# Kernel tuning notes

Measured on AMD Instinct MI355X. Metric: run time of the kernel, lower is better.

## Reference

```python
import jax, jax.numpy as jnp
import numpy as np

N_NODES, N_EDGES, F_IN = 8192, 32768, 16
N_SUB, N_GRAPH = 512, 32
EDGE_DIM, HID = 5, 128
DIMS = [(16, 32), (32, 64), (64, 64)]  # (M_in, M_out) per NNConv layer


def _segment_mean(x, seg, n):
    s = jax.ops.segment_sum(x, seg, num_segments=n)
    c = jax.ops.segment_sum(jnp.ones((x.shape[0], 1), x.dtype), seg, num_segments=n)
    return s / jnp.maximum(c, 1.0)


def _nnconv(x, src, dst, eattr, W1, b1, W2, b2, root, bias):
    # edge MLP -> per-edge weight matrix theta: [E, M_in, M_out]
    h = jax.nn.relu(eattr @ W1 + b1)
    theta = (h @ W2 + b2).reshape(-1, x.shape[1], root.shape[1])
    msg = jnp.einsum('ei,eio->eo', x[src], theta)          # gather + per-edge matvec
    agg = jax.ops.segment_sum(msg, dst, num_segments=x.shape[0])  # scatter-add (aggr='add')
    return agg + x @ root + bias


def setup_inputs() -> dict:
    key = jax.random.key(0)
    ks = jax.random.split(key, 32)
    inp = {}
    inp['x'] = jax.random.normal(ks[0], (N_NODES, F_IN), jnp.float32)
    inp['edge_index'] = jax.random.randint(ks[1], (2, N_EDGES), 0, N_NODES)
    inp['edge_attr'] = jax.random.uniform(ks[2], (N_EDGES, EDGE_DIM), jnp.float32)
    inp['node_to_subgraph'] = jnp.sort(jax.random.randint(ks[3], (N_NODES,), 0, N_SUB))
    inp['subgraph_to_graph'] = jnp.sort(jax.random.randint(ks[4], (N_SUB,), 0, N_GRAPH))
    i = 5
    for l, (ci, co) in enumerate(DIMS):
        inp[f'W1_{l}'] = jax.random.normal(ks[i], (EDGE_DIM, HID), jnp.float32) * 0.1
        inp[f'b1_{l}'] = jnp.zeros((HID,), jnp.float32)
        inp[f'W2_{l}'] = jax.random.normal(ks[i + 1], (HID, ci * co), jnp.float32) * 0.05
        inp[f'b2_{l}'] = jnp.zeros((ci * co,), jnp.float32)
        inp[f'root_{l}'] = jax.random.normal(ks[i + 2], (ci, co), jnp.float32) * 0.1
        inp[f'bias_{l}'] = jnp.zeros((co,), jnp.float32)
        i += 3
    inp['fc1_w'] = jax.random.normal(ks[i], (64, 32), jnp.float32) * 0.1
    inp['fc1_b'] = jnp.zeros((32,), jnp.float32)
    inp['fc2_w'] = jax.random.normal(ks[i + 1], (32, 16), jnp.float32) * 0.1
    inp['fc2_b'] = jnp.zeros((16,), jnp.float32)
    inp['fc3_w'] = jax.random.normal(ks[i + 2], (16, 1), jnp.float32) * 0.1
    inp['fc3_b'] = jnp.zeros((1,), jnp.float32)
    return inp


def reference(x, edge_index, edge_attr, node_to_subgraph, subgraph_to_graph,
              W1_0, b1_0, W2_0, b2_0, root_0, bias_0,
              W1_1, b1_1, W2_1, b2_1, root_1, bias_1,
              W1_2, b1_2, W2_2, b2_2, root_2, bias_2,
              fc1_w, fc1_b, fc2_w, fc2_b, fc3_w, fc3_b):
    src, dst = edge_index[0], edge_index[1]
    layers = [(W1_0, b1_0, W2_0, b2_0, root_0, bias_0),
              (W1_1, b1_1, W2_1, b2_1, root_1, bias_1),
              (W1_2, b1_2, W2_2, b2_2, root_2, bias_2)]
    h = x
    for (W1, b1, W2, b2, root, bias) in layers:
        h = jax.nn.elu(_nnconv(h, src, dst, edge_attr, W1, b1, W2, b2, root, bias))
    h = _segment_mean(h, node_to_subgraph, N_SUB)      # global_mean_pool over subgraphs
    h = _segment_mean(h, subgraph_to_graph, N_GRAPH)   # global_mean_pool over graphs
    h = jax.nn.elu(h @ fc1_w + fc1_b)
    h = jax.nn.elu(h @ fc2_w + fc2_b)
    return (h @ fc3_w + fc3_b).reshape(-1)
```

## Files before the change

### kernel.cpp

```cpp
#include <hip/hip_runtime.h>

#define E_EDGES 32768
#define NN 8192
#define HID 128

typedef _Float16 half8 __attribute__((ext_vector_type(8)));
typedef _Float16 half4 __attribute__((ext_vector_type(4)));
typedef float f32x4 __attribute__((ext_vector_type(4)));

__device__ __forceinline__ void prep_one(int idx, int l2ci, int l2co,
                                         const float* __restrict__ W2,
                                         const float* __restrict__ b2,
                                         _Float16* __restrict__ out) {
  int CI = 1 << l2ci, CO = 1 << l2co;
  int Kmain = CI << 7;
  int j = idx & 7;
  int n = (idx >> 3) & (CO - 1);
  int kg = idx >> (3 + l2co);
  int k = kg * 8 + j;
  float v = 0.f;
  if (k < Kmain) {
    int hh = k >> l2ci, i = k & (CI - 1);
    v = W2[((hh << l2ci) + i) * CO + n];
  } else if (k < Kmain + CI) {
    v = b2[(k - Kmain) * CO + n];
  }
  out[idx] = (_Float16)v;
}

#define ZTOT (8192 * 32 + 8192 * 64 + 8192 * 64 + 512 * 64 + 512)
#define PREP0 (2176 * 32)
#define PREP1 (4224 * 64)
#define PREP2 (8320 * 64)

__global__ void prep_k(float* __restrict__ zr,
                       const float* __restrict__ W2a, const float* __restrict__ b2a, _Float16* __restrict__ oa,
                       const float* __restrict__ W2b, const float* __restrict__ b2b, _Float16* __restrict__ ob,
                       const float* __restrict__ W2c, const float* __restrict__ b2c, _Float16* __restrict__ oc) {
  int idx = blockIdx.x * 256 + threadIdx.x;
  if (idx < ZTOT) { zr[idx] = 0.f; return; }
  idx -= ZTOT;
  if (idx < PREP0) prep_one(idx, 4, 5, W2a, b2a, oa);
  else if (idx < PREP0 + PREP1) prep_one(idx - PREP0, 5, 6, W2b, b2b, ob);
  else if (idx < PREP0 + PREP1 + PREP2) prep_one(idx - PREP0 - PREP1, 6, 6, W2c, b2c, oc);
}

template <int CI, int CO>
__launch_bounds__(256, 4)
__global__ void msg_mfma_k(const float* __restrict__ xcur, const int* __restrict__ src,
                           const int* __restrict__ dst, const float* __restrict__ eattr,
                           const float* __restrict__ W1, const float* __restrict__ b1,
                           const _Float16* __restrict__ Bsw, float* __restrict__ agg) {
  constexpr int ME = 128;
  constexpr int L2CI = (CI == 64) ? 6 : ((CI == 32) ? 5 : 4);
  constexpr int XSTR = CI + 8;
  constexpr int FC = CO / 16;
  constexpr int C4 = CI / 4;
  constexpr int L2C4 = L2CI - 2;
  constexpr int NV = (CI == 64) ? 2 : 1;
  constexpr int HS = 40;
  constexpr int CW = CI / 4;
  constexpr int NP = CW / 2;

  __shared__ _Float16 he_t[ME * HS];
  __shared__ _Float16 xs_s[ME * XSTR];
  __shared__ float ea_s[ME * 5];
  __shared__ float W1s[5 * 32];
  __shared__ float b1s[32];
  __shared__ int src_s[ME];
  __shared__ int dst_s[ME];

  int t = threadIdx.x;
  int e0 = blockIdx.x * ME;
  int y = blockIdx.y;
  int hbeg = y * 32;

  for (int j = t; j < ME * 5; j += 256) ea_s[j] = eattr[e0 * 5 + j];
  if (t < 5 * 32) W1s[t] = W1[(t >> 5) * HID + hbeg + (t & 31)];
  if (t < 32) b1s[t] = b1[hbeg + t];
  if (t < ME) { src_s[t] = src[e0 + t]; dst_s[t] = dst[e0 + t]; }
  __syncthreads();

  for (int j = t; j < 32 * ME; j += 256) {
    int hl = j >> 7, e = j & (ME - 1);
    float v = b1s[hl];
#pragma unroll
    for (int d = 0; d < 5; ++d) v += ea_s[e * 5 + d] * W1s[d * 32 + hl];
    he_t[e * HS + hl] = (_Float16)fmaxf(v, 0.f);
  }
  for (int j = t; j < ME * C4; j += 256) {
    int e = j >> L2C4, i4 = j & (C4 - 1);
    float4 v = ((const float4*)xcur)[src_s[e] * C4 + i4];
    half4 hq = {(_Float16)v.x, (_Float16)v.y, (_Float16)v.z, (_Float16)v.w};
    *(half4*)&xs_s[e * XSTR + i4 * 4] = hq;
  }
  __syncthreads();

  int lane = t & 63;
  int w = t >> 6;
  int quad = lane >> 4, l15 = lane & 15;
  int hsel = (quad >> 1) & 1;

  half8 xreg[2][NV];
#pragma unroll
  for (int fr = 0; fr < 2; ++fr)
#pragma unroll
    for (int v = 0; v < NV; ++v)
      xreg[fr][v] = *(const half8*)&xs_s[(w * 32 + fr * 16 + l15) * XSTR +
                                         ((quad * 8 + v * 32) & (CI - 1))];

  int cbeg = y * CI;
  int TC = CI + ((y == 3) ? 4 : 0);

  const half8* bsw8 = (const half8*)Bsw;
  int ib = quad * CO + l15;

  f32x4 acc[2][FC];
#pragma unroll
  for (int fr = 0; fr < 2; ++fr)
#pragma unroll
    for (int fc = 0; fc < FC; ++fc)
#pragma unroll
      for (int r = 0; r < 4; ++r) acc[fr][fc][r] = 0.f;

  half8 breg[2][FC];
#pragma unroll
  for (int p = 0; p < 2; ++p)
#pragma unroll
    for (int fc = 0; fc < FC; ++fc)
      breg[p][fc] = bsw8[(cbeg + p) * 4 * CO + ib + fc * 16];

  for (int win = 0; win < 4; ++win) {
    half8 hreg[2];
#pragma unroll
    for (int fr = 0; fr < 2; ++fr)
      hreg[fr] = *(const half8*)&he_t[(w * 32 + fr * 16 + l15) * HS + win * 8];
    for (int cl2 = 0; cl2 < NP; ++cl2) {
#pragma unroll
      for (int p = 0; p < 2; ++p) {
        int cl = win * CW + cl2 * 2 + p;
        int vi = (CI == 64) ? p : 0;
        half8 a[2];
#pragma unroll
        for (int fr = 0; fr < 2; ++fr) {
          _Float16 hv;
          if (CI == 16)      hv = hreg[fr][2 * (cl2 * 2 + p) + hsel];
          else if (CI == 32) hv = hreg[fr][cl2 * 2 + p];
          else               hv = hreg[fr][cl2];
          half8 hb = {hv, hv, hv, hv, hv, hv, hv, hv};
          a[fr] = xreg[fr][vi] * hb;
        }
#pragma unroll
        for (int fc = 0; fc < FC; ++fc) {
#pragma unroll
          for (int fr = 0; fr < 2; ++fr)
            acc[fr][fc] = __builtin_amdgcn_mfma_f32_16x16x32_f16(a[fr], breg[p][fc], acc[fr][fc], 0, 0, 0);
        }
        int cn = cl + 2;
        if (cn >= TC) cn = TC - 1;
#pragma unroll
        for (int fc = 0; fc < FC; ++fc)
          breg[p][fc] = bsw8[(cbeg + cn) * 4 * CO + ib + fc * 16];
      }
    }
  }

  if (y == 3) {
#pragma unroll
    for (int j = 0; j < 4; ++j) {
      int cl = CI + j;
      int p = j & 1;
      int vi = (CI == 64) ? p : 0;
#pragma unroll
      for (int fc = 0; fc < FC; ++fc) {
#pragma unroll
        for (int fr = 0; fr < 2; ++fr)
          acc[fr][fc] = __builtin_amdgcn_mfma_f32_16x16x32_f16(xreg[fr][vi], breg[p][fc], acc[fr][fc], 0, 0, 0);
      }
      int cn = cl + 2;
      if (cn >= TC) cn = TC - 1;
#pragma unroll
      for (int fc = 0; fc < FC; ++fc)
        breg[p][fc] = bsw8[(cbeg + cn) * 4 * CO + ib + fc * 16];
    }
  }

#pragma unroll
  for (int fr = 0; fr < 2; ++fr)
#pragma unroll
    for (int r = 0; r < 4; ++r) {
      int el = w * 32 + fr * 16 + quad * 4 + r;
      int d = dst_s[el];
      float* base = agg + (size_t)d * CO + l15;
#pragma unroll
      for (int fc = 0; fc < FC; ++fc)
        atomicAdd(base + fc * 16, acc[fr][fc][r]);
    }
}

template <int CI, int CO, bool POOL, bool CNT>
__global__ void fin_k(const float* __restrict__ xcur, const float* __restrict__ root,
                      const float* __restrict__ bias, const float* __restrict__ agg,
                      const int* __restrict__ n2s, int* __restrict__ cnt_sub,
                      float* __restrict__ ssum, float* __restrict__ xnext) {
  constexpr int NB = 256 / CO;
  __shared__ float xs[NB * CI];
  int t = threadIdx.x;
  int n0 = blockIdx.x * NB;
  for (int j = t; j < NB * CI; j += 256) xs[j] = xcur[n0 * CI + j];
  __syncthreads();
  int nl = t / CO, o = t & (CO - 1);
  int n = n0 + nl;
  float a = bias[o] + agg[n * CO + o];
#pragma unroll
  for (int i = 0; i < CI; ++i) a += xs[nl * CI + i] * root[i * CO + o];
  float r = a > 0.f ? a : expm1f(a);
  if (CNT && o == 0) atomicAdd(&cnt_sub[n2s[n]], 1);
  if (POOL) atomicAdd(&ssum[(n2s[n] << 6) + o], r);
  else xnext[n * CO + o] = r;
}

__device__ __forceinline__ int lbound(const int* __restrict__ a, int n, int v) {
  int lo = 0, hi = n;
  while (lo < hi) { int m = (lo + hi) >> 1; if (a[m] < v) lo = m + 1; else hi = m; }
  return lo;
}

__global__ void head_k(const float* __restrict__ ssum, const int* __restrict__ cnt_sub,
                       const int* __restrict__ s2g,
                       const float* __restrict__ w1, const float* __restrict__ b1,
                       const float* __restrict__ w2, const float* __restrict__ b2,
                       const float* __restrict__ w3, const float* __restrict__ b3,
                       float* __restrict__ out) {
  int g = blockIdx.x;
  int t = threadIdx.x;
  __shared__ float m[64], s1[32], s2[16];
  int slo = lbound(s2g, 512, g);
  int shi = lbound(s2g, 512, g + 1);
  float acc = 0.f;
  for (int s = slo; s < shi; ++s)
    acc += ssum[(s << 6) + t] / fmaxf((float)cnt_sub[s], 1.f);
  m[t] = acc / fmaxf((float)(shi - slo), 1.f);
  __syncthreads();
  if (t < 32) {
    float a = b1[t];
    for (int i = 0; i < 64; ++i) a += m[i] * w1[i * 32 + t];
    s1[t] = a > 0.f ? a : expm1f(a);
  }
  __syncthreads();
  if (t < 16) {
    float a = b2[t];
    for (int i = 0; i < 32; ++i) a += s1[i] * w2[i * 16 + t];
    s2[t] = a > 0.f ? a : expm1f(a);
  }
  __syncthreads();
  if (t == 0) {
    float a = b3[0];
    for (int i = 0; i < 16; ++i) a += s2[i] * w3[i];
    out[g] = a;
  }
}

extern "C" void kernel_launch(void* const* d_in, const int* in_sizes, int n_in,
                              void* d_out, int out_size, void* d_ws, size_t ws_size,
                              hipStream_t stream) {
  (void)in_sizes; (void)n_in; (void)out_size; (void)ws_size;
  const float* x0 = (const float*)d_in[0];
  const int* ei = (const int*)d_in[1];
  const float* ea = (const float*)d_in[2];
  const int* n2s = (const int*)d_in[3];
  const int* s2g = (const int*)d_in[4];
  const float* W1_[3] = {(const float*)d_in[5], (const float*)d_in[11], (const float*)d_in[17]};
  const float* b1_[3] = {(const float*)d_in[6], (const float*)d_in[12], (const float*)d_in[18]};
  const float* W2_[3] = {(const float*)d_in[7], (const float*)d_in[13], (const float*)d_in[19]};
  const float* b2_[3] = {(const float*)d_in[8], (const float*)d_in[14], (const float*)d_in[20]};
  const float* rt_[3] = {(const float*)d_in[9], (const float*)d_in[15], (const float*)d_in[21]};
  const float* bs_[3] = {(const float*)d_in[10], (const float*)d_in[16], (const float*)d_in[22]};
  const float* fc1w = (const float*)d_in[23]; const float* fc1b = (const float*)d_in[24];
  const float* fc2w = (const float*)d_in[25]; const float* fc2b = (const float*)d_in[26];
  const float* fc3w = (const float*)d_in[27]; const float* fc3b = (const float*)d_in[28];
  float* out = (float*)d_out;

  const int* srcp = ei;
  const int* dstp = ei + E_EDGES;

  char* wsb = (char*)d_ws;
  size_t off = 0;
  auto alloc = [&](size_t bytes) {
    void* p = wsb + off;
    off += (bytes + 255) & ~(size_t)255;
    return p;
  };
  _Float16* Bsw0 = (_Float16*)alloc((size_t)PREP0 * 2);
  _Float16* Bsw1 = (_Float16*)alloc((size_t)PREP1 * 2);
  _Float16* Bsw2 = (_Float16*)alloc((size_t)PREP2 * 2);
  float* agg1 = (float*)alloc((size_t)NN * 32 * 4);
  float* agg2 = (float*)alloc((size_t)NN * 64 * 4);
  float* agg3 = (float*)alloc((size_t)NN * 64 * 4);
  float* ssum = (float*)alloc((size_t)512 * 64 * 4);
  int* cnt_sub = (int*)alloc((size_t)512 * 4);
  float* x1 = (float*)alloc((size_t)NN * 32 * 4);
  float* x2 = (float*)alloc((size_t)NN * 64 * 4);

  const int preptot = ZTOT + PREP0 + PREP1 + PREP2;
  prep_k<<<(preptot + 255) / 256, 256, 0, stream>>>(agg1, W2_[0], b2_[0], Bsw0,
                                                    W2_[1], b2_[1], Bsw1,
                                                    W2_[2], b2_[2], Bsw2);

  dim3 mg(E_EDGES / 128, 4);
  msg_mfma_k<16, 32><<<mg, 256, 0, stream>>>(x0, srcp, dstp, ea, W1_[0], b1_[0], Bsw0, agg1);
  fin_k<16, 32, false, true><<<NN / 8, 256, 0, stream>>>(x0, rt_[0], bs_[0], agg1, n2s, cnt_sub, ssum, x1);
  msg_mfma_k<32, 64><<<mg, 256, 0, stream>>>(x1, srcp, dstp, ea, W1_[1], b1_[1], Bsw1, agg2);
  fin_k<32, 64, false, false><<<NN / 4, 256, 0, stream>>>(x1, rt_[1], bs_[1], agg2, n2s, cnt_sub, ssum, x2);
  msg_mfma_k<64, 64><<<mg, 256, 0, stream>>>(x2, srcp, dstp, ea, W1_[2], b1_[2], Bsw2, agg3);
  fin_k<64, 64, true, false><<<NN / 4, 256, 0, stream>>>(x2, rt_[2], bs_[2], agg3, n2s, cnt_sub, ssum, nullptr);

  head_k<<<32, 64, 0, stream>>>(ssum, cnt_sub, s2g, fc1w, fc1b, fc2w, fc2b, fc3w, fc3b, out);
}
```

Measured before the change: 281.6 us.

## Enlarge per-block edge tile to 512 and restage B layout per split

```diff
diff --git a/kernel.cpp b/kernel.cpp
--- a/kernel.cpp
+++ b/kernel.cpp
@@ -5,33 +5,37 @@
 #define HID 128
 
 typedef _Float16 half8 __attribute__((ext_vector_type(8)));
-typedef _Float16 half4 __attribute__((ext_vector_type(4)));
 typedef float f32x4 __attribute__((ext_vector_type(4)));
 
-__device__ __forceinline__ void prep_one(int idx, int l2ci, int l2co,
+#define S0 (4 * 22 * 1024)
+#define S1 (4 * 38 * 2048)
+#define S2 (4 * 70 * 2048)
+#define ZTOT (8192 * 32 + 8192 * 64 + 8192 * 64 + 512 * 64 + 512)
+
+__device__ __forceinline__ void prep_one(int idx, int l2ci, int l2co, int tcp2,
                                          const float* __restrict__ W2,
                                          const float* __restrict__ b2,
                                          _Float16* __restrict__ out) {
   int CI = 1 << l2ci, CO = 1 << l2co;
-  int Kmain = CI << 7;
-  int j = idx & 7;
-  int n = (idx >> 3) & (CO - 1);
-  int kg = idx >> (3 + l2co);
-  int k = kg * 8 + j;
+  int CH = 32 * CO;
+  int per_split = tcp2 * CH;
+  int y = idx / per_split;
+  int r = idx - y * per_split;
+  int cl = r / CH;
+  int m = r & (CH - 1);
+  int j = m & 7, l15 = (m >> 3) & 15, quad = (m >> 7) & 3, fc = m >> 9;
+  int kl = cl * 32 + quad * 8 + j;
+  int n = fc * 16 + l15;
+  int kmain = 32 * CI;
   float v = 0.f;
-  if (k < Kmain) {
-    int hh = k >> l2ci, i = k & (CI - 1);
-    v = W2[((hh << l2ci) + i) * CO + n];
-  } else if (k < Kmain + CI) {
-    v = b2[(k - Kmain) * CO + n];
+  if (kl < kmain) {
+    int h = y * 32 + (kl >> l2ci), i = kl & (CI - 1);
+    v = W2[(h * CI + i) * CO + n];
+  } else if (y == 3 && kl < kmain + CI) {
+    v = b2[(kl - kmain) * CO + n];
   }
   out[idx] = (_Float16)v;
 }
-
-#define ZTOT (8192 * 32 + 8192 * 64 + 8192 * 64 + 512 * 64 + 512)
-#define PREP0 (2176 * 32)
-#define PREP1 (4224 * 64)
-#define PREP2 (8320 * 64)
 
 __global__ void prep_k(float* __restrict__ zr,
                        const float* __restrict__ W2a, const float* __restrict__ b2a, _Float16* __restrict__ oa,
@@ -40,30 +44,28 @@
   int idx = blockIdx.x * 256 + threadIdx.x;
   if (idx < ZTOT) { zr[idx] = 0.f; return; }
   idx -= ZTOT;
-  if (idx < PREP0) prep_one(idx, 4, 5, W2a, b2a, oa);
-  else if (idx < PREP0 + PREP1) prep_one(idx - PREP0, 5, 6, W2b, b2b, ob);
-  else if (idx < PREP0 + PREP1 + PREP2) prep_one(idx - PREP0 - PREP1, 6, 6, W2c, b2c, oc);
+  if (idx < S0) { prep_one(idx, 4, 5, 22, W2a, b2a, oa); return; }
+  idx -= S0;
+  if (idx < S1) { prep_one(idx, 5, 6, 38, W2b, b2b, ob); return; }
+  idx -= S1;
+  if (idx < S2) prep_one(idx, 6, 6, 70, W2c, b2c, oc);
 }
 
 template <int CI, int CO>
-__launch_bounds__(256, 4)
+__launch_bounds__(256, 1)
 __global__ void msg_mfma_k(const float* __restrict__ xcur, const int* __restrict__ src,
                            const int* __restrict__ dst, const float* __restrict__ eattr,
                            const float* __restrict__ W1, const float* __restrict__ b1,
                            const _Float16* __restrict__ Bsw, float* __restrict__ agg) {
-  constexpr int ME = 128;
-  constexpr int L2CI = (CI == 64) ? 6 : ((CI == 32) ? 5 : 4);
-  constexpr int XSTR = CI + 8;
+  constexpr int ME = 512;
   constexpr int FC = CO / 16;
-  constexpr int C4 = CI / 4;
-  constexpr int L2C4 = L2CI - 2;
+  constexpr int CH8 = 4 * CO;
+  constexpr int TCP = (CI == 64) ? 68 : ((CI == 32) ? 36 : 20);
+  constexpr int CW = (CI == 64) ? 16 : ((CI == 32) ? 8 : 4);
   constexpr int NV = (CI == 64) ? 2 : 1;
   constexpr int HS = 40;
-  constexpr int CW = CI / 4;
-  constexpr int NP = CW / 2;
-
-  __shared__ _Float16 he_t[ME * HS];
-  __shared__ _Float16 xs_s[ME * XSTR];
+
+  __shared__ __align__(16) _Float16 he_t[ME * HS];
   __shared__ float ea_s[ME * 5];
   __shared__ float W1s[5 * 32];
   __shared__ float b1s[32];
@@ -76,120 +78,113 @@
   int hbeg = y * 32;
 
   for (int j = t; j < ME * 5; j += 256) ea_s[j] = eattr[e0 * 5 + j];
-  if (t < 5 * 32) W1s[t] = W1[(t >> 5) * HID + hbeg + (t & 31)];
+  if (t < 160) W1s[t] = W1[(t >> 5) * HID + hbeg + (t & 31)];
   if (t < 32) b1s[t] = b1[hbeg + t];
-  if (t < ME) { src_s[t] = src[e0 + t]; dst_s[t] = dst[e0 + t]; }
+  src_s[t] = src[e0 + t]; src_s[t + 256] = src[e0 + 256 + t];
+  dst_s[t] = dst[e0 + t]; dst_s[t + 256] = dst[e0 + 256 + t];
   __syncthreads();
 
   for (int j = t; j < 32 * ME; j += 256) {
-    int hl = j >> 7, e = j & (ME - 1);
+    int hl = j >> 9, e = j & (ME - 1);
     float v = b1s[hl];
 #pragma unroll
     for (int d = 0; d < 5; ++d) v += ea_s[e * 5 + d] * W1s[d * 32 + hl];
     he_t[e * HS + hl] = (_Float16)fmaxf(v, 0.f);
-  }
-  for (int j = t; j < ME * C4; j += 256) {
-    int e = j >> L2C4, i4 = j & (C4 - 1);
-    float4 v = ((const float4*)xcur)[src_s[e] * C4 + i4];
-    half4 hq = {(_Float16)v.x, (_Float16)v.y, (_Float16)v.z, (_Float16)v.w};
-    *(half4*)&xs_s[e * XSTR + i4 * 4] = hq;
   }
   __syncthreads();
 
   int lane = t & 63;
   int w = t >> 6;
   int quad = lane >> 4, l15 = lane & 15;
-  int hsel = (quad >> 1) & 1;
-
-  half8 xreg[2][NV];
-#pragma unroll
-  for (int fr = 0; fr < 2; ++fr)
-#pragma unroll
-    for (int v = 0; v < NV; ++v)
-      xreg[fr][v] = *(const half8*)&xs_s[(w * 32 + fr * 16 + l15) * XSTR +
-                                         ((quad * 8 + v * 32) & (CI - 1))];
-
-  int cbeg = y * CI;
-  int TC = CI + ((y == 3) ? 4 : 0);
-
-  const half8* bsw8 = (const half8*)Bsw;
-  int ib = quad * CO + l15;
-
-  f32x4 acc[2][FC];
-#pragma unroll
-  for (int fr = 0; fr < 2; ++fr)
+  int hsel = quad >> 1;
+  int qoff = quad * 16 + l15;
+
+  half8 xreg[8][NV];
+  const float4* xp = (const float4*)xcur;
+#pragma unroll
+  for (int fr = 0; fr < 8; ++fr) {
+    int e = w * 128 + fr * 16 + l15;
+    int row = src_s[e];
+#pragma unroll
+    for (int v = 0; v < NV; ++v) {
+      int i0 = (quad * 8 + v * 32) & (CI - 1);
+      float4 aa = xp[row * (CI / 4) + i0 / 4];
+      float4 bb = xp[row * (CI / 4) + i0 / 4 + 1];
+      half8 h = {(_Float16)aa.x, (_Float16)aa.y, (_Float16)aa.z, (_Float16)aa.w,
+                 (_Float16)bb.x, (_Float16)bb.y, (_Float16)bb.z, (_Float16)bb.w};
+      xreg[fr][v] = h;
+    }
+  }
+
+  f32x4 acc[8][FC];
+#pragma unroll
+  for (int fr = 0; fr < 8; ++fr)
 #pragma unroll
     for (int fc = 0; fc < FC; ++fc)
 #pragma unroll
       for (int r = 0; r < 4; ++r) acc[fr][fc][r] = 0.f;
 
+  const half8* bs8 = (const half8*)Bsw + (size_t)y * (TCP + 2) * CH8;
+
   half8 breg[2][FC];
 #pragma unroll
   for (int p = 0; p < 2; ++p)
 #pragma unroll
     for (int fc = 0; fc < FC; ++fc)
-      breg[p][fc] = bsw8[(cbeg + p) * 4 * CO + ib + fc * 16];
-
+      breg[p][fc] = bs8[(size_t)p * CH8 + fc * 64 + qoff];
+
+#pragma unroll 1
   for (int win = 0; win < 4; ++win) {
-    half8 hreg[2];
-#pragma unroll
-    for (int fr = 0; fr < 2; ++fr)
-      hreg[fr] = *(const half8*)&he_t[(w * 32 + fr * 16 + l15) * HS + win * 8];
-    for (int cl2 = 0; cl2 < NP; ++cl2) {
-#pragma unroll
-      for (int p = 0; p < 2; ++p) {
-        int cl = win * CW + cl2 * 2 + p;
-        int vi = (CI == 64) ? p : 0;
-        half8 a[2];
-#pragma unroll
-        for (int fr = 0; fr < 2; ++fr) {
-          _Float16 hv;
-          if (CI == 16)      hv = hreg[fr][2 * (cl2 * 2 + p) + hsel];
-          else if (CI == 32) hv = hreg[fr][cl2 * 2 + p];
-          else               hv = hreg[fr][cl2];
-          half8 hb = {hv, hv, hv, hv, hv, hv, hv, hv};
-          a[fr] = xreg[fr][vi] * hb;
-        }
-#pragma unroll
-        for (int fc = 0; fc < FC; ++fc) {
-#pragma unroll
-          for (int fr = 0; fr < 2; ++fr)
-            acc[fr][fc] = __builtin_amdgcn_mfma_f32_16x16x32_f16(a[fr], breg[p][fc], acc[fr][fc], 0, 0, 0);
-        }
-        int cn = cl + 2;
-        if (cn >= TC) cn = TC - 1;
-#pragma unroll
-        for (int fc = 0; fc < FC; ++fc)
-          breg[p][fc] = bsw8[(cbeg + cn) * 4 * CO + ib + fc * 16];
+    half8 hregw[8];
+#pragma unroll
+    for (int fr = 0; fr < 8; ++fr)
+      hregw[fr] = *(const half8*)&he_t[(w * 128 + fr * 16 + l15) * HS + win * 8];
+    const half8* bw8 = bs8 + (size_t)win * CW * CH8;
+#pragma unroll
+    for (int cc = 0; cc < CW; ++cc) {
+      int p = cc & 1;
+      int vi = (CI == 64) ? (cc & 1) : 0;
+      half8 a[8];
+#pragma unroll
+      for (int fr = 0; fr < 8; ++fr) {
+        _Float16 hv;
+        if (CI == 64)      hv = hregw[fr][cc >> 1];
+        else if (CI == 32) hv = hregw[fr][cc];
+        else               hv = hregw[fr][cc * 2 + hsel];
+        half8 hb = {hv, hv, hv, hv, hv, hv, hv, hv};
+        a[fr] = xreg[fr][vi] * hb;
       }
+#pragma unroll
+      for (int fc = 0; fc < FC; ++fc)
+#pragma unroll
+        for (int fr = 0; fr < 8; ++fr)
+          acc[fr][fc] = __builtin_amdgcn_mfma_f32_16x16x32_f16(a[fr], breg[p][fc], acc[fr][fc], 0, 0, 0);
+#pragma unroll
+      for (int fc = 0; fc < FC; ++fc)
+        breg[p][fc] = bw8[(size_t)(cc + 2) * CH8 + fc * 64 + qoff];
     }
   }
 
-  if (y == 3) {
-#pragma unroll
-    for (int j = 0; j < 4; ++j) {
-      int cl = CI + j;
-      int p = j & 1;
-      int vi = (CI == 64) ? p : 0;
-#pragma unroll
-      for (int fc = 0; fc < FC; ++fc) {
-#pragma unroll
-        for (int fr = 0; fr < 2; ++fr)
-          acc[fr][fc] = __builtin_amdgcn_mfma_f32_16x16x32_f16(xreg[fr][vi], breg[p][fc], acc[fr][fc], 0, 0, 0);
-      }
-      int cn = cl + 2;
-      if (cn >= TC) cn = TC - 1;
-#pragma unroll
-      for (int fc = 0; fc < FC; ++fc)
-        breg[p][fc] = bsw8[(cbeg + cn) * 4 * CO + ib + fc * 16];
-    }
-  }
-
-#pragma unroll
-  for (int fr = 0; fr < 2; ++fr)
+  const half8* bt8 = bs8 + (size_t)CI * CH8;
+#pragma unroll
+  for (int j = 0; j < TCP - CI; ++j) {
+    int p = j & 1;
+    int vi = (CI == 64) ? (j & 1) : 0;
+#pragma unroll
+    for (int fc = 0; fc < FC; ++fc)
+#pragma unroll
+      for (int fr = 0; fr < 8; ++fr)
+        acc[fr][fc] = __builtin_amdgcn_mfma_f32_16x16x32_f16(xreg[fr][vi], breg[p][fc], acc[fr][fc], 0, 0, 0);
+#pragma unroll
+    for (int fc = 0; fc < FC; ++fc)
+      breg[p][fc] = bt8[(size_t)(j + 2) * CH8 + fc * 64 + qoff];
+  }
+
+#pragma unroll
+  for (int fr = 0; fr < 8; ++fr)
 #pragma unroll
     for (int r = 0; r < 4; ++r) {
-      int el = w * 32 + fr * 16 + quad * 4 + r;
+      int el = w * 128 + fr * 16 + quad * 4 + r;
       int d = dst_s[el];
       float* base = agg + (size_t)d * CO + l15;
 #pragma unroll
@@ -291,9 +286,9 @@
     off += (bytes + 255) & ~(size_t)255;
     return p;
   };
-  _Float16* Bsw0 = (_Float16*)alloc((size_t)PREP0 * 2);
-  _Float16* Bsw1 = (_Float16*)alloc((size_t)PREP1 * 2);
-  _Float16* Bsw2 = (_Float16*)alloc((size_t)PREP2 * 2);
+  _Float16* Bsw0 = (_Float16*)alloc((size_t)S0 * 2);
+  _Float16* Bsw1 = (_Float16*)alloc((size_t)S1 * 2);
+  _Float16* Bsw2 = (_Float16*)alloc((size_t)S2 * 2);
   float* agg1 = (float*)alloc((size_t)NN * 32 * 4);
   float* agg2 = (float*)alloc((size_t)NN * 64 * 4);
   float* agg3 = (float*)alloc((size_t)NN * 64 * 4);
@@ -302,12 +297,12 @@
   float* x1 = (float*)alloc((size_t)NN * 32 * 4);
   float* x2 = (float*)alloc((size_t)NN * 64 * 4);
 
-  const int preptot = ZTOT + PREP0 + PREP1 + PREP2;
+  const int preptot = ZTOT + S0 + S1 + S2;
   prep_k<<<(preptot + 255) / 256, 256, 0, stream>>>(agg1, W2_[0], b2_[0], Bsw0,
                                                     W2_[1], b2_[1], Bsw1,
                                                     W2_[2], b2_[2], Bsw2);
 
-  dim3 mg(E_EDGES / 128, 4);
+  dim3 mg(E_EDGES / 512, 4);
   msg_mfma_k<16, 32><<<mg, 256, 0, stream>>>(x0, srcp, dstp, ea, W1_[0], b1_[0], Bsw0, agg1);
   fin_k<16, 32, false, true><<<NN / 8, 256, 0, stream>>>(x0, rt_[0], bs_[0], agg1, n2s, cnt_sub, ssum, x1);
   msg_mfma_k<32, 64><<<mg, 256, 0, stream>>>(x1, srcp, dstp, ea, W1_[1], b1_[1], Bsw1, agg2);
```

Result: slower. 331.9 us (+17.8%).
